# Performance work log

Hardware: AMD Instinct MI355X
Metric: run time of the kernel (lower is better)

## Reference

```python
import jax, jax.numpy as jnp
import numpy as np

MARGIN = 0.4
SCALE = 80.0
NEG_FILL = -1e30  # used instead of -inf for masked logsumexp (keeps grads NaN-free)

N, D, NUM_CLASSES = 8192, 128, 512


def setup_inputs() -> dict:
    key = jax.random.key(0)
    k1, k2 = jax.random.split(key)
    embeds = jax.random.normal(k1, (N, D), dtype=jnp.float32)
    labels = jax.random.randint(k2, (N,), 0, NUM_CLASSES, dtype=jnp.int64)
    return {"embeds": embeds, "labels": labels}


def _masked_lse(terms, mask):
    # stable logsumexp over axis=1 restricted to mask
    t = jnp.where(mask, terms, NEG_FILL)
    m = jnp.max(t, axis=1, keepdims=True)
    return jnp.squeeze(m, 1) + jnp.log(jnp.sum(jnp.exp(t - m), axis=1))


def reference(embeds, labels):
    # L2-normalize embeddings (F.normalize, p=2, dim=1, eps=1e-12)
    norm = jnp.maximum(jnp.linalg.norm(embeds, axis=1, keepdims=True), 1e-12)
    e = embeds / norm
    sim = e @ e.T  # [N, N]

    same = labels[:, None] == labels[None, :]
    eye = jnp.eye(labels.shape[0], dtype=bool)
    pos_mask = same & ~eye          # positives for each anchor (row)
    neg_mask = ~same                # negatives for each anchor

    # alphas are computed under no_grad in the original
    ap_alpha = jax.lax.stop_gradient(jax.nn.relu(1.0 + MARGIN - sim))
    an_alpha = jax.lax.stop_gradient(jax.nn.relu(sim + MARGIN))

    ap_term = -SCALE * ap_alpha * (sim - 1.0 + MARGIN)
    an_term = SCALE * an_alpha * (sim - MARGIN)

    np_cnt = jnp.sum(pos_mask, axis=1)  # positives per anchor
    nn_cnt = jnp.sum(neg_mask, axis=1)  # negatives per anchor
    valid = (np_cnt > 0) & (nn_cnt > 0)

    # All-triplets logsumexp factorizes: LSE over (p,n) pairs of ap_term[p]
    # equals LSE over p + log(num_neg); symmetric for an_term.
    lse_p = _masked_lse(ap_term, pos_mask)
    lse_n = _masked_lse(an_term, neg_mask)
    log_np = jnp.where(valid, jnp.log(np_cnt.astype(sim.dtype)), 0.0)
    log_nn = jnp.where(valid, jnp.log(nn_cnt.astype(sim.dtype)), 0.0)

    loss_i = jax.nn.softplus(lse_p + log_nn + lse_n + log_np)
    loss = jnp.sum(jnp.where(valid, loss_i, 0.0)) / jnp.maximum(
        jnp.sum(valid).astype(sim.dtype), 1.0)
    return loss
```

## Files before the change

kernel.cpp:

```cpp
#include <hip/hip_runtime.h>
#include <hip/hip_bf16.h>

#define NN_ 8192
#define DD_ 128
#define NCLS 512
#define NSPLIT 16
#define JSPLIT (NN_ / NSPLIT)

typedef short bf16x8 __attribute__((ext_vector_type(8)));
typedef float f32x4 __attribute__((ext_vector_type(4)));

union U4 { uint4 u; bf16x8 h; };

#if __has_builtin(__builtin_amdgcn_exp2f)
#define EXP2(x) __builtin_amdgcn_exp2f(x)
#else
#define EXP2(x) __expf((x) * 0.69314718056f)
#endif

#define C1 115.415603f
#define C2 96.9491065f
#define LN2 0.69314718056f

__device__ __forceinline__ unsigned short f2bf(float f) {
    unsigned int u = __float_as_uint(f);
    unsigned int r = (u + 0x7FFFu + ((u >> 16) & 1u)) >> 16;
    return (unsigned short)r;
}


__global__ __launch_bounds__(512) void k_zero(int* __restrict__ hist) {
    hist[threadIdx.x] = 0;
}

__global__ __launch_bounds__(256) void k_hist(const int* __restrict__ labels,
                                              int* __restrict__ hist) {
    int i = blockIdx.x * 256 + threadIdx.x;
    atomicAdd(&hist[labels[i]], 1);
}

__global__ __launch_bounds__(512) void k_scan(const int* __restrict__ hist,
                                              int* __restrict__ start,
                                              int* __restrict__ base) {
    __shared__ int wsum[8];
    int t = threadIdx.x;
    int v = hist[t];
    int x = v;
#pragma unroll
    for (int m = 1; m < 64; m <<= 1) {
        int y = __shfl_up(x, m);
        if ((t & 63) >= m) x += y;
    }
    if ((t & 63) == 63) wsum[t >> 6] = x;
    __syncthreads();
    int w = t >> 6, woff = 0;
#pragma unroll
    for (int k = 0; k < 8; k++)
        if (k < w) woff += wsum[k];
    int excl = woff + x - v;
    start[t] = excl;
    base[t] = excl;
    if (t == 0) start[NCLS] = NN_;
}

__global__ __launch_bounds__(256) void k_scatter(const int* __restrict__ labels,
                                                 int* __restrict__ base,
                                                 int* __restrict__ srcrow,
                                                 int* __restrict__ plab) {
    int row = blockIdx.x * 256 + threadIdx.x;
    int l = labels[row];
    int p = atomicAdd(&base[l], 1);
    srcrow[p] = row;
    plab[p] = l;
}

__global__ __launch_bounds__(256) void k_norm(const float* __restrict__ x,
                                              const int* __restrict__ srcrow,
                                              unsigned short* __restrict__ ebf) {
    int t = threadIdx.x;
    int r16 = t >> 4;
    int g = t & 15;
    int slot = blockIdx.x * 16 + r16;
    int orig = srcrow[slot];
    const float4* xr = (const float4*)(x + (size_t)orig * DD_);
    float4 v0 = xr[g * 2];
    float4 v1 = xr[g * 2 + 1];
    float ss = v0.x * v0.x + v0.y * v0.y + v0.z * v0.z + v0.w * v0.w +
               v1.x * v1.x + v1.y * v1.y + v1.z * v1.z + v1.w * v1.w;
#pragma unroll
    for (int m = 1; m < 16; m <<= 1) ss += __shfl_xor(ss, m);
    float inv = 1.0f / fmaxf(sqrtf(ss), 1e-12f);
    float vs[8] = {v0.x, v0.y, v0.z, v0.w, v1.x, v1.y, v1.z, v1.w};
    unsigned int p[4];
#pragma unroll
    for (int k = 0; k < 4; k++) {
        unsigned short lo = f2bf(vs[2 * k] * inv);
        unsigned short hi = f2bf(vs[2 * k + 1] * inv);
        p[k] = (unsigned int)lo | ((unsigned int)hi << 16);
    }
    uint4 out = {p[0], p[1], p[2], p[3]};
    ((uint4*)ebf)[blockIdx.x * 256 + g * 16 + r16] = out;
}

__global__ __launch_bounds__(512, 4) void k_main(const unsigned short* __restrict__ ebf,
                                                 const int* __restrict__ plab,
                                                 const int* __restrict__ start,
                                                 float* __restrict__ states) {
    __shared__ uint4 bsh[1024];

    const int tid = threadIdx.x;
    const int lane = tid & 63;
    const int wave = tid >> 6;
    const int quad = lane >> 4;
    const int lcol = lane & 15;
    const int rowbase = blockIdx.y * 256 + wave * 32;
    const int jsplit = blockIdx.x;
    const int j0 = jsplit * JSPLIT;

    const uint4* fb = (const uint4*)ebf;

    U4 afr[2][4];
#pragma unroll
    for (int g = 0; g < 2; g++)
#pragma unroll
        for (int kc = 0; kc < 4; kc++)
            afr[g][kc].u = fb[((rowbase >> 4) + g) * 256 + kc * 64 + lane];

    int il[2][4];
#pragma unroll
    for (int g = 0; g < 2; g++)
#pragma unroll
        for (int r = 0; r < 4; r++) il[g][r] = plab[rowbase + g * 16 + quad * 4 + r];

    int labmin = __builtin_amdgcn_readfirstlane(plab[rowbase]);
    int labmax = __builtin_amdgcn_readfirstlane(plab[rowbase + 31]);
    int lo = __builtin_amdgcn_readfirstlane(start[labmin]);
    int hi = __builtin_amdgcn_readfirstlane(start[labmax + 1]);

    float S_an[2][4], m_p[2][4], s_p[2][4], cnt[2][4];
#pragma unroll
    for (int g = 0; g < 2; g++)
#pragma unroll
        for (int r = 0; r < 4; r++) {
            S_an[g][r] = 0.f;
            m_p[g][r] = -1e30f;
            s_p[g][r] = 0.f;
            cnt[g][r] = 0.f;
        }

    bsh[tid] = fb[(j0 >> 4) * 256 + tid];
    __syncthreads();

    const int NIT = JSPLIT / 32;
    for (int it = 0; it < NIT; ++it) {
        const int cur = it & 1;
        const int jt = j0 + it * 32;
        const bool has = (it + 1 < NIT);

        uint4 stg;
        if (has) stg = fb[((jt + 32) >> 4) * 256 + tid];

        const int bb = (cur << 9) + lane;

#pragma unroll
        for (int c = 0; c < 2; c++) {
            U4 bf[4];
#pragma unroll
            for (int kc = 0; kc < 4; kc++) bf[kc].u = bsh[bb + c * 256 + kc * 64];
            f32x4 acc0 = {0.f, 0.f, 0.f, 0.f};
            f32x4 acc1 = {0.f, 0.f, 0.f, 0.f};
#pragma unroll
            for (int kc = 0; kc < 4; kc++) {
                acc0 = __builtin_amdgcn_mfma_f32_16x16x32_bf16(afr[0][kc].h, bf[kc].h, acc0, 0, 0, 0);
                acc1 = __builtin_amdgcn_mfma_f32_16x16x32_bf16(afr[1][kc].h, bf[kc].h, acc1, 0, 0, 0);
            }
            const int jc = jt + c * 16;
            if (jc < hi && jc + 16 > lo) {
                int jl = plab[jc + lcol];
                int j = jc + lcol;
#pragma unroll
                for (int g = 0; g < 2; g++) {
#pragma unroll
                    for (int r = 0; r < 4; r++) {
                        float s = (g == 0) ? acc0[r] : acc1[r];
                        int i = rowbase + g * 16 + quad * 4 + r;
                        bool same = (jl == il[g][r]);
                        float a = fmaxf(s + 0.4f, 0.0f);
                        float e = EXP2(fmaf(a * C1, s - 0.4f, -C2));
                        S_an[g][r] += same ? 0.0f : e;
                        cnt[g][r] += same ? 1.0f : 0.0f;
                        if (same && j != i) {
                            float al = fmaxf(1.4f - s, 0.0f) * (-C1);
                            float tp = al * (s - 0.6f);
                            float mn = fmaxf(m_p[g][r], tp);
                            s_p[g][r] = s_p[g][r] * EXP2(m_p[g][r] - mn) + EXP2(tp - mn);
                            m_p[g][r] = mn;
                        }
                    }
                }
            } else {
#pragma unroll
                for (int r = 0; r < 4; r++) {
                    float s0 = acc0[r];
                    float a0 = fmaxf(s0 + 0.4f, 0.0f);
                    S_an[0][r] += EXP2(fmaf(a0 * C1, s0 - 0.4f, -C2));
                    float s1 = acc1[r];
                    float a1 = fmaxf(s1 + 0.4f, 0.0f);
                    S_an[1][r] += EXP2(fmaf(a1 * C1, s1 - 0.4f, -C2));
                }
            }
        }

        if (has) bsh[(cur ^ 1) * 512 + tid] = stg;
        __syncthreads();
    }

#pragma unroll
    for (int g = 0; g < 2; g++)
#pragma unroll
        for (int r = 0; r < 4; r++) {
#pragma unroll
            for (int m = 1; m < 16; m <<= 1) {
                S_an[g][r] += __shfl_xor(S_an[g][r], m);
                cnt[g][r] += __shfl_xor(cnt[g][r], m);
                float m2 = __shfl_xor(m_p[g][r], m);
                float s2 = __shfl_xor(s_p[g][r], m);
                float mn = fmaxf(m_p[g][r], m2);
                s_p[g][r] = s_p[g][r] * EXP2(m_p[g][r] - mn) + s2 * EXP2(m2 - mn);
                m_p[g][r] = mn;
            }
        }
    if (lcol == 0) {
#pragma unroll
        for (int g = 0; g < 2; g++)
#pragma unroll
            for (int r = 0; r < 4; r++) {
                int i = rowbase + g * 16 + quad * 4 + r;
                float4 st = {m_p[g][r], s_p[g][r], S_an[g][r], cnt[g][r]};
                ((float4*)states)[(size_t)i * NSPLIT + jsplit] = st;
            }
    }
}

__global__ __launch_bounds__(256) void k_fin(const float* __restrict__ states,
                                             float* __restrict__ partials) {
    int i = blockIdx.x * 256 + threadIdx.x;
    float m_p = -1e30f, s_p = 0.f, S_an = 0.f, cnt = 0.f;
#pragma unroll
    for (int k = 0; k < NSPLIT; k++) {
        float4 st = ((const float4*)states)[(size_t)i * NSPLIT + k];
        S_an += st.z;
        cnt += st.w;
        float mn = fmaxf(m_p, st.x);
        s_p = s_p * EXP2(m_p - mn) + st.y * EXP2(st.x - mn);
        m_p = mn;
    }
    int np = (int)cnt - 1;
    int nn = NN_ - (int)cnt;
    float loss = 0.0f, v = 0.0f;
    if (np > 0 && nn > 0 && s_p > 0.f && S_an > 0.f) {
        float lse_p = LN2 * m_p + __logf(s_p);
        float lse_n = 67.2f + __logf(S_an);
        float z = lse_p + lse_n + __logf((float)np) + __logf((float)nn);
        loss = fmaxf(z, 0.0f) + log1pf(__expf(-fabsf(z)));
        v = 1.0f;
    }
#pragma unroll
    for (int m = 1; m < 64; m <<= 1) {
        loss += __shfl_xor(loss, m);
        v += __shfl_xor(v, m);
    }
    if ((threadIdx.x & 63) == 0) {
        int w = (blockIdx.x << 2) | (threadIdx.x >> 6);
        partials[w * 2] = loss;
        partials[w * 2 + 1] = v;
    }
}

__global__ void k_div(const float* __restrict__ partials, float* __restrict__ out) {
    int t = threadIdx.x;
    float loss = partials[t * 2] + partials[(t + 64) * 2];
    float v = partials[t * 2 + 1] + partials[(t + 64) * 2 + 1];
#pragma unroll
    for (int m = 1; m < 64; m <<= 1) {
        loss += __shfl_xor(loss, m);
        v += __shfl_xor(v, m);
    }
    if (t == 0) out[0] = loss / fmaxf(v, 1.0f);
}

extern "C" void kernel_launch(void* const* d_in, const int* in_sizes, int n_in,
                              void* d_out, int out_size, void* d_ws, size_t ws_size,
                              hipStream_t stream) {
    const float* embeds = (const float*)d_in[0];
    const int* labels = (const int*)d_in[1];
    float* out = (float*)d_out;

    char* ws = (char*)d_ws;
    unsigned short* ebf = (unsigned short*)ws;
    float* states = (float*)(ws + 2097152);
    float* partials = (float*)(ws + 4194304);
    int* srcrow = (int*)(ws + 4195328);
    int* plab = (int*)(ws + 4228096);
    int* start = (int*)(ws + 4260864);
    int* base = (int*)(ws + 4263168);
    int* hist = (int*)(ws + 4265216);

    k_zero<<<1, NCLS, 0, stream>>>(hist);
    k_hist<<<NN_ / 256, 256, 0, stream>>>(labels, hist);
    k_scan<<<1, NCLS, 0, stream>>>(hist, start, base);
    k_scatter<<<NN_ / 256, 256, 0, stream>>>(labels, base, srcrow, plab);
    k_norm<<<NN_ / 16, 256, 0, stream>>>(embeds, srcrow, ebf);
    k_main<<<dim3(NSPLIT, NN_ / 256), 512, 0, stream>>>(ebf, plab, start, states);
    k_fin<<<NN_ / 256, 256, 0, stream>>>(states, partials);
    k_div<<<1, 64, 0, stream>>>(partials, out);
}
```

Baseline: 111.7 us.

## Double column split count, process 64 columns per iteration, simplify negative exponent

Doubles the number of column splits so twice as many workgroups run the main similarity kernel. Each loop iteration now stages 64 columns instead of 32, using a larger shared buffer, which halves the number of barriers per tile. The negative-term exponent is rewritten algebraically as C1*(u^2-1) with u=max(s,-0.4), saving an add per element. The per-split state buffer doubles, so workspace offsets move and the finalize pass reads more partial states.

```diff
diff --git a/kernel.cpp b/kernel.cpp
--- a/kernel.cpp
+++ b/kernel.cpp
@@ -4,7 +4,7 @@
 #define NN_ 8192
 #define DD_ 128
 #define NCLS 512
-#define NSPLIT 16
+#define NSPLIT 32
 #define JSPLIT (NN_ / NSPLIT)
 
 typedef short bf16x8 __attribute__((ext_vector_type(8)));
@@ -106,7 +106,7 @@
                                                  const int* __restrict__ plab,
                                                  const int* __restrict__ start,
                                                  float* __restrict__ states) {
-    __shared__ uint4 bsh[1024];
+    __shared__ uint4 bsh[2048];
 
     const int tid = threadIdx.x;
     const int lane = tid & 63;
@@ -148,25 +148,33 @@
             cnt[g][r] = 0.f;
         }
 
-    bsh[tid] = fb[(j0 >> 4) * 256 + tid];
+    {
+        const int tb = (j0 >> 4) * 256;
+        bsh[tid] = fb[tb + tid];
+        bsh[tid + 512] = fb[tb + tid + 512];
+    }
     __syncthreads();
 
-    const int NIT = JSPLIT / 32;
+    const int NIT = JSPLIT / 64;
     for (int it = 0; it < NIT; ++it) {
         const int cur = it & 1;
-        const int jt = j0 + it * 32;
+        const int jt = j0 + it * 64;
         const bool has = (it + 1 < NIT);
 
-        uint4 stg;
-        if (has) stg = fb[((jt + 32) >> 4) * 256 + tid];
-
-        const int bb = (cur << 9) + lane;
-
-#pragma unroll
-        for (int c = 0; c < 2; c++) {
+        uint4 stg0, stg1;
+        if (has) {
+            const int tn = ((jt + 64) >> 4) * 256;
+            stg0 = fb[tn + tid];
+            stg1 = fb[tn + tid + 512];
+        }
+
+        const int bbase = (cur << 10) + lane;
+
+#pragma unroll
+        for (int c = 0; c < 4; c++) {
             U4 bf[4];
 #pragma unroll
-            for (int kc = 0; kc < 4; kc++) bf[kc].u = bsh[bb + c * 256 + kc * 64];
+            for (int kc = 0; kc < 4; kc++) bf[kc].u = bsh[bbase + c * 256 + kc * 64];
             f32x4 acc0 = {0.f, 0.f, 0.f, 0.f};
             f32x4 acc1 = {0.f, 0.f, 0.f, 0.f};
 #pragma unroll
@@ -185,8 +193,8 @@
                         float s = (g == 0) ? acc0[r] : acc1[r];
                         int i = rowbase + g * 16 + quad * 4 + r;
                         bool same = (jl == il[g][r]);
-                        float a = fmaxf(s + 0.4f, 0.0f);
-                        float e = EXP2(fmaf(a * C1, s - 0.4f, -C2));
+                        float u = fmaxf(s, -0.4f);
+                        float e = EXP2(fmaf(u * C1, u, -C1));
                         S_an[g][r] += same ? 0.0f : e;
                         cnt[g][r] += same ? 1.0f : 0.0f;
                         if (same && j != i) {
@@ -201,17 +209,18 @@
             } else {
 #pragma unroll
                 for (int r = 0; r < 4; r++) {
-                    float s0 = acc0[r];
-                    float a0 = fmaxf(s0 + 0.4f, 0.0f);
-                    S_an[0][r] += EXP2(fmaf(a0 * C1, s0 - 0.4f, -C2));
-                    float s1 = acc1[r];
-                    float a1 = fmaxf(s1 + 0.4f, 0.0f);
-                    S_an[1][r] += EXP2(fmaf(a1 * C1, s1 - 0.4f, -C2));
+                    float u0 = fmaxf(acc0[r], -0.4f);
+                    S_an[0][r] += EXP2(fmaf(u0 * C1, u0, -C1));
+                    float u1 = fmaxf(acc1[r], -0.4f);
+                    S_an[1][r] += EXP2(fmaf(u1 * C1, u1, -C1));
                 }
             }
         }
 
-        if (has) bsh[(cur ^ 1) * 512 + tid] = stg;
+        if (has) {
+            bsh[((cur ^ 1) << 10) + tid] = stg0;
+            bsh[((cur ^ 1) << 10) + tid + 512] = stg1;
+        }
         __syncthreads();
     }
 
@@ -299,12 +308,12 @@
     char* ws = (char*)d_ws;
     unsigned short* ebf = (unsigned short*)ws;
     float* states = (float*)(ws + 2097152);
-    float* partials = (float*)(ws + 4194304);
-    int* srcrow = (int*)(ws + 4195328);
-    int* plab = (int*)(ws + 4228096);
-    int* start = (int*)(ws + 4260864);
-    int* base = (int*)(ws + 4263168);
-    int* hist = (int*)(ws + 4265216);
+    float* partials = (float*)(ws + 6291456);
+    int* srcrow = (int*)(ws + 6292480);
+    int* plab = (int*)(ws + 6325248);
+    int* start = (int*)(ws + 6358016);
+    int* base = (int*)(ws + 6360068);
+    int* hist = (int*)(ws + 6362116);
 
     k_zero<<<1, NCLS, 0, stream>>>(hist);
     k_hist<<<NN_ / 256, 256, 0, stream>>>(labels, hist);
```

Measured after the change: 114.3 us. 1.02x slower.
